# Performance work log

Measured on AMD Instinct MI355X. Metric: run time of the kernel, lower is better.

## Reference

```python
import jax, jax.numpy as jnp
import numpy as np
import math

B, S, D, H = 4, 2048, 1024, 16
DH = D // H  # 64


def setup_inputs() -> dict:
    key = jax.random.key(0)
    ks = jax.random.split(key, 7)
    scale = 1.0 / math.sqrt(D)
    q = jax.random.normal(ks[0], (B, S, D), dtype=jnp.float32)
    k = jax.random.normal(ks[1], (B, S, D), dtype=jnp.float32)
    v = jax.random.normal(ks[2], (B, S, D), dtype=jnp.float32)
    mask = jnp.tril(jnp.ones((S, S), dtype=jnp.int32))[None, None]  # [1,1,S,S] causal
    wq = jax.random.normal(ks[3], (D, D), dtype=jnp.float32) * scale
    wk = jax.random.normal(ks[4], (D, D), dtype=jnp.float32) * scale
    wv = jax.random.normal(ks[5], (D, D), dtype=jnp.float32) * scale
    wo = jax.random.normal(ks[6], (D, D), dtype=jnp.float32) * scale
    return {"q": q, "k": k, "v": v, "mask": mask, "wq": wq, "wk": wk, "wv": wv, "wo": wo}


def reference(q, k, v, mask, wq, wk, wv, wo):
    # nn.Linear(bias=False): y = x @ W.T
    qry = q @ wq.T
    key = k @ wk.T
    val = v @ wv.T
    # [B,S,D] -> [B,H,S,DH]
    qry = qry.reshape(B, S, H, DH).transpose(0, 2, 1, 3)
    key = key.reshape(B, S, H, DH).transpose(0, 2, 1, 3)
    val = val.reshape(B, S, H, DH).transpose(0, 2, 1, 3)
    scores = jnp.einsum('bhqd,bhkd->bhqk', qry, key) / math.sqrt(DH)
    scores = jnp.where(mask == 0, jnp.float32(-1e9), scores)
    attn = jax.nn.softmax(scores, axis=-1)  # dropout p=0.0 -> identity
    x = jnp.einsum('bhqk,bhkd->bhqd', attn, val)
    x = x.transpose(0, 2, 1, 3).reshape(B, S, D)
    return x @ wo.T
```

## Files before the change

### kernel.cpp

```cpp
#include <hip/hip_runtime.h>
#include <hip/hip_bf16.h>

typedef __attribute__((ext_vector_type(8))) short bf16x8;
typedef __attribute__((ext_vector_type(4))) float f32x4;
typedef __attribute__((ext_vector_type(16))) float f32x16;

#define MFMA16(a, b, c) __builtin_amdgcn_mfma_f32_16x16x32_bf16((a), (b), (c), 0, 0, 0)
#define MFMA32(a, b, c) __builtin_amdgcn_mfma_f32_32x32x16_bf16((a), (b), (c), 0, 0, 0)

#if defined(__has_builtin)
#if __has_builtin(__builtin_amdgcn_exp2f)
#define EXP2(x) __builtin_amdgcn_exp2f(x)
#endif
#endif
#ifndef EXP2
#define EXP2(x) exp2f(x)
#endif

__device__ __forceinline__ short f2b(float f) {
  unsigned u = __builtin_bit_cast(unsigned, f);
  u += 0x7FFFu + ((u >> 16) & 1u);
  return (short)(u >> 16);
}
__device__ __forceinline__ unsigned cvtpk(float lo, float hi) {
  unsigned r;
  asm("v_cvt_pk_bf16_f32 %0, %1, %2" : "=v"(r) : "v"(lo), "v"(hi));
  return r;
}

__global__ __launch_bounds__(256) void cvt_bf16(const float* __restrict__ s,
                                                short* __restrict__ d, int n8) {
  int i = blockIdx.x * 256 + threadIdx.x;
  if (i >= n8) return;
  const float4* sp = (const float4*)s;
  float4 a = sp[2 * i], b = sp[2 * i + 1];
  bf16x8 o;
  o[0] = f2b(a.x); o[1] = f2b(a.y); o[2] = f2b(a.z); o[3] = f2b(a.w);
  o[4] = f2b(b.x); o[5] = f2b(b.y); o[6] = f2b(b.z); o[7] = f2b(b.w);
  *(bf16x8*)(d + (long)i * 8) = o;
}

template <int MODE>
__global__ __launch_bounds__(256) void gemm_bt(const short* __restrict__ A,
                                               const short* __restrict__ BT,
                                               void* __restrict__ Cout,
                                               int M, int N, int K, float oscale) {
  __shared__ __align__(16) short As[128 * 64];
  __shared__ __align__(16) short Bs[128 * 64];
  const int t = threadIdx.x;
  const int l = t & 63, w = t >> 6;
  const int grp = l >> 4, li = l & 15;
  const int nbn = N >> 7;
  const int bm = (int)blockIdx.x / nbn, bn = (int)blockIdx.x % nbn;
  const int m0 = bm << 7, n0 = bn << 7;
  const int wm = (w >> 1) << 6, wn = (w & 1) << 6;
  const int srow = t >> 3, scol = (t & 7) << 3;
  f32x4 acc[4][4] = {};
  for (int kt = 0; kt < K; kt += 64) {
#pragma unroll
    for (int i = 0; i < 4; ++i) {
      const short* ga = A + (long)(m0 + i * 32 + srow) * K + kt + scol;
      __builtin_amdgcn_global_load_lds(
          (const __attribute__((address_space(1))) void*)ga,
          (__attribute__((address_space(3))) void*)&As[i * 2048 + t * 8], 16, 0, 0);
    }
#pragma unroll
    for (int i = 0; i < 4; ++i) {
      const short* gb = BT + (long)(n0 + i * 32 + srow) * K + kt + scol;
      __builtin_amdgcn_global_load_lds(
          (const __attribute__((address_space(1))) void*)gb,
          (__attribute__((address_space(3))) void*)&Bs[i * 2048 + t * 8], 16, 0, 0);
    }
    __syncthreads();
#pragma unroll
    for (int kk = 0; kk < 64; kk += 32) {
      bf16x8 af[4], bfr[4];
#pragma unroll
      for (int mi = 0; mi < 4; ++mi)
        af[mi] = *(const bf16x8*)&As[(wm + mi * 16 + li) * 64 + kk + grp * 8];
#pragma unroll
      for (int ni = 0; ni < 4; ++ni)
        bfr[ni] = *(const bf16x8*)&Bs[(wn + ni * 16 + li) * 64 + kk + grp * 8];
#pragma unroll
      for (int mi = 0; mi < 4; ++mi)
#pragma unroll
        for (int ni = 0; ni < 4; ++ni)
          acc[mi][ni] = MFMA16(af[mi], bfr[ni], acc[mi][ni]);
    }
    __syncthreads();
  }
#pragma unroll
  for (int mi = 0; mi < 4; ++mi) {
#pragma unroll
    for (int ni = 0; ni < 4; ++ni) {
      f32x4 v = acc[mi][ni];
      int n = n0 + wn + ni * 16 + li;
#pragma unroll
      for (int r = 0; r < 4; ++r) {
        int m = m0 + wm + mi * 16 + grp * 4 + r;
        if (MODE == 2) {
          ((float*)Cout)[(long)m * N + n] = v[r];
        } else {
          int b = m >> 11, sq = m & 2047;
          int h = n >> 6, dh = n & 63;
          if (MODE == 0)
            ((short*)Cout)[(((long)(b * 16 + h) * 2048 + sq) << 6) + dh] = f2b(v[r] * oscale);
          else
            ((short*)Cout)[(((long)(b * 16 + h) * 64 + dh) << 11) + sq] = f2b(v[r] * oscale);
        }
      }
    }
  }
}

__device__ __forceinline__ void attn_tile(const short* Kbuf, const short* Vbuf,
                                          const bf16x8 qf[4], f32x16& oa, f32x16& ob,
                                          float& mrun, float& lsum, int kt, bool diag,
                                          int khmax, int qg, int q, int hi) {
  f32x16 p0 = {}, p1 = {};
  __builtin_amdgcn_s_setprio(1);
#pragma unroll
  for (int kd = 0; kd < 4; ++kd) {
    int colB = kd * 32 + hi * 16;
    bf16x8 kf0 = *(const bf16x8*)((const char*)Kbuf + q * 128 + (colB ^ ((q & 7) << 4)));
    p0 = MFMA32(kf0, qf[kd], p0);
  }
  if (khmax == 2) {
#pragma unroll
    for (int kd = 0; kd < 4; ++kd) {
      int colB = kd * 32 + hi * 16;
      bf16x8 kf1 = *(const bf16x8*)((const char*)Kbuf + (q + 32) * 128 + (colB ^ ((q & 7) << 4)));
      p1 = MFMA32(kf1, qf[kd], p1);
    }
  }
  __builtin_amdgcn_s_setprio(0);
  if (diag) {
#pragma unroll
    for (int r = 0; r < 16; ++r) {
      int key0 = kt * 64 + (r & 3) + 8 * (r >> 2) + 4 * hi;
      if (key0 > qg) p0[r] = -1e30f;
      if (key0 + 32 > qg) p1[r] = -1e30f;
    }
  }
  float pm = p0[0];
#pragma unroll
  for (int r = 1; r < 16; ++r) pm = fmaxf(pm, p0[r]);
  if (khmax == 2) {
#pragma unroll
    for (int r = 0; r < 16; ++r) pm = fmaxf(pm, p1[r]);
  }
  pm = fmaxf(pm, __shfl_xor(pm, 32));
  const bool skip = __all(pm - mrun <= 11.5f);
  float mn;
  float alpha = 1.f;
  if (skip) {
    mn = mrun;
  } else {
    mn = fmaxf(mrun, pm);
    alpha = EXP2(mrun - mn);
    mrun = mn;
  }
  float ts = 0.f;
#pragma unroll
  for (int r = 0; r < 16; ++r) { p0[r] = EXP2(p0[r] - mn); ts += p0[r]; }
  if (khmax == 2) {
#pragma unroll
    for (int r = 0; r < 16; ++r) { p1[r] = EXP2(p1[r] - mn); ts += p1[r]; }
  }
  ts += __shfl_xor(ts, 32);
  if (skip) {
    lsum += ts;
  } else {
    lsum = lsum * alpha + ts;
#pragma unroll
    for (int r = 0; r < 16; ++r) { oa[r] *= alpha; ob[r] *= alpha; }
  }
  unsigned own0[8], prt0[8], own1[8], prt1[8];
#pragma unroll
  for (int g = 0; g < 4; ++g) {
    own0[2 * g]     = cvtpk(p0[4 * g], p0[4 * g + 1]);
    own0[2 * g + 1] = cvtpk(p0[4 * g + 2], p0[4 * g + 3]);
  }
#pragma unroll
  for (int i = 0; i < 8; ++i) prt0[i] = __shfl_xor(own0[i], 32);
  if (khmax == 2) {
#pragma unroll
    for (int g = 0; g < 4; ++g) {
      own1[2 * g]     = cvtpk(p1[4 * g], p1[4 * g + 1]);
      own1[2 * g + 1] = cvtpk(p1[4 * g + 2], p1[4 * g + 3]);
    }
#pragma unroll
    for (int i = 0; i < 8; ++i) prt1[i] = __shfl_xor(own1[i], 32);
  }
  __builtin_amdgcn_s_setprio(1);
#define PVSTEP(KD, OWN, PRT)                                                              \
  {                                                                                       \
    const int kdl = (KD) & 1;                                                             \
    unsigned b0 = hi ? PRT[4 * kdl + 2] : OWN[4 * kdl];                                   \
    unsigned b1 = hi ? PRT[4 * kdl + 3] : OWN[4 * kdl + 1];                               \
    unsigned b2 = hi ? OWN[4 * kdl + 2] : PRT[4 * kdl];                                   \
    unsigned b3 = hi ? OWN[4 * kdl + 3] : PRT[4 * kdl + 1];                               \
    int4 bi = {(int)b0, (int)b1, (int)b2, (int)b3};                                       \
    bf16x8 pb = __builtin_bit_cast(bf16x8, bi);                                           \
    int colB = (KD) * 32 + hi * 16;                                                       \
    bf16x8 vf0 = *(const bf16x8*)((const char*)Vbuf + q * 128 + (colB ^ ((q & 7) << 4))); \
    bf16x8 vf1 = *(const bf16x8*)((const char*)Vbuf + (q + 32) * 128 + (colB ^ ((q & 7) << 4))); \
    oa = MFMA32(vf0, pb, oa);                                                             \
    ob = MFMA32(vf1, pb, ob);                                                             \
  }
  PVSTEP(0, own0, prt0);
  PVSTEP(1, own0, prt0);
  if (khmax == 2) {
    PVSTEP(2, own1, prt1);
    PVSTEP(3, own1, prt1);
  }
#undef PVSTEP
  __builtin_amdgcn_s_setprio(0);
}

__global__ __launch_bounds__(256, 2) void attn_fwd(const short* __restrict__ Qh,
                                                   const short* __restrict__ Kh,
                                                   const short* __restrict__ Vt,
                                                   short* __restrict__ Xb) {
  __shared__ __align__(16) short Ks[2][4096];
  __shared__ __align__(16) short Vs[2][4096];
  const int bh = blockIdx.x;
  const int qtA = blockIdx.y;
  const int qtB = 15 - qtA;
  const int t = threadIdx.x, l = t & 63, w = t >> 6;
  const int q = l & 31, hi = l >> 5;
  const int q0wA = qtA * 128 + w * 32, q0wB = qtB * 128 + w * 32;
  const int qgA = q0wA + q, qgB = q0wB + q;
  const short* Qp = Qh + (long)bh * 131072;
  const char* Kb = (const char*)(Kh + (long)bh * 131072);
  const char* Vb = (const char*)(Vt + (long)bh * 131072);

  bf16x8 qfA[4], qfB[4];
#pragma unroll
  for (int kd = 0; kd < 4; ++kd) {
    qfA[kd] = *(const bf16x8*)(Qp + (long)qgA * 64 + kd * 16 + hi * 8);
    qfB[kd] = *(const bf16x8*)(Qp + (long)qgB * 64 + kd * 16 + hi * 8);
  }

  const int co0 = t * 16, co1 = co0 + 4096;

  f32x16 oaA = {}, obA = {}, oaB = {}, obB = {};
  float mrunA = -1e30f, lsumA = 0.f, mrunB = -1e30f, lsumB = 0.f;
  const int tripsA = (q0wA >> 6) + 1;
  const int tripsB = (q0wB >> 6) + 1;
  const int nt = 2 * qtB + 2;

#define STAGE(KT, BUF)                                                                   \
  {                                                                                      \
    long ktb = (long)(KT) * 8192;                                                        \
    _Pragma("unroll") for (int c = 0; c < 2; ++c) {                                      \
      int o = c ? co1 : co0;                                                             \
      int ksrc = o ^ (((o >> 7) & 7) << 4);                                              \
      __builtin_amdgcn_global_load_lds(                                                  \
          (const __attribute__((address_space(1))) void*)(Kb + ktb + ksrc),              \
          (__attribute__((address_space(3))) void*)((char*)Ks[BUF] + o), 16, 0, 0);      \
      int row = o >> 7, c16 = (o >> 4) & 7;                                              \
      int vsrc = row * 4096 + (KT) * 128 + (((c16 ^ (row & 7))) << 4);                   \
      __builtin_amdgcn_global_load_lds(                                                  \
          (const __attribute__((address_space(1))) void*)(Vb + vsrc),                    \
          (__attribute__((address_space(3))) void*)((char*)Vs[BUF] + o), 16, 0, 0);      \
    }                                                                                    \
  }

  STAGE(0, 0);
  __syncthreads();

  for (int kt = 0; kt < nt; ++kt) {
    const int buf = kt & 1;
    if (kt + 1 < nt) STAGE(kt + 1, buf ^ 1);

    if (kt < tripsB) {
      const bool diag = (kt == tripsB - 1);
      const int khmax = (diag && ((q0wB & 32) == 0)) ? 1 : 2;
      attn_tile(Ks[buf], Vs[buf], qfB, oaB, obB, mrunB, lsumB, kt, diag, khmax, qgB, q, hi);
    }
    if (kt < tripsA) {
      const bool diag = (kt == tripsA - 1);
      const int khmax = (diag && ((q0wA & 32) == 0)) ? 1 : 2;
      attn_tile(Ks[buf], Vs[buf], qfA, oaA, obA, mrunA, lsumA, kt, diag, khmax, qgA, q, hi);
    }
    __syncthreads();
  }

  const int b = bh >> 4, h = bh & 15;
#define EPI(OA, OB, LS, QG)                                                \
  {                                                                        \
    const float inv = 1.f / (LS);                                          \
    short* orow = Xb + (long)(b * 2048 + (QG)) * 1024 + h * 64;            \
    _Pragma("unroll") for (int g = 0; g < 4; ++g) {                        \
      unsigned u0 = cvtpk((OA)[4 * g] * inv, (OA)[4 * g + 1] * inv);       \
      unsigned u1 = cvtpk((OA)[4 * g + 2] * inv, (OA)[4 * g + 3] * inv);   \
      uint2 uu = {u0, u1};                                                 \
      *(uint2*)(orow + 8 * g + 4 * hi) = uu;                               \
      unsigned w0 = cvtpk((OB)[4 * g] * inv, (OB)[4 * g + 1] * inv);       \
      unsigned w1 = cvtpk((OB)[4 * g + 2] * inv, (OB)[4 * g + 3] * inv);   \
      uint2 ww = {w0, w1};                                                 \
      *(uint2*)(orow + 32 + 8 * g + 4 * hi) = ww;                          \
    }                                                                      \
  }
  EPI(oaA, obA, lsumA, qgA);
  EPI(oaB, obB, lsumB, qgB);
#undef EPI
}

extern "C" void kernel_launch(void* const* d_in, const int* in_sizes, int n_in,
                              void* d_out, int out_size, void* d_ws, size_t ws_size,
                              hipStream_t stream) {
  const float* q  = (const float*)d_in[0];
  const float* k  = (const float*)d_in[1];
  const float* v  = (const float*)d_in[2];
  const float* wq = (const float*)d_in[4];
  const float* wk = (const float*)d_in[5];
  const float* wv = (const float*)d_in[6];
  const float* wo = (const float*)d_in[7];

  short* ws = (short*)d_ws;
  const long T = 8388608;
  short* qb  = ws;
  short* kb  = qb + T;
  short* vb  = kb + T;
  short* Qh  = vb + T;
  short* Kh  = Qh + T;
  short* Vt  = Kh + T;
  short* Xb  = Vt + T;
  short* wqb = Xb + T;
  short* wkb = wqb + 1048576;
  short* wvb = wkb + 1048576;
  short* wob = wvb + 1048576;

  cvt_bf16<<<4096, 256, 0, stream>>>(q, qb, 1048576);
  cvt_bf16<<<4096, 256, 0, stream>>>(k, kb, 1048576);
  cvt_bf16<<<4096, 256, 0, stream>>>(v, vb, 1048576);
  cvt_bf16<<<512, 256, 0, stream>>>(wq, wqb, 131072);
  cvt_bf16<<<512, 256, 0, stream>>>(wk, wkb, 131072);
  cvt_bf16<<<512, 256, 0, stream>>>(wv, wvb, 131072);
  cvt_bf16<<<512, 256, 0, stream>>>(wo, wob, 131072);

  gemm_bt<0><<<512, 256, 0, stream>>>(qb, wqb, (void*)Qh, 8192, 1024, 1024, 0.18033688f);
  gemm_bt<0><<<512, 256, 0, stream>>>(kb, wkb, (void*)Kh, 8192, 1024, 1024, 1.0f);
  gemm_bt<1><<<512, 256, 0, stream>>>(vb, wvb, (void*)Vt, 8192, 1024, 1024, 1.0f);
  attn_fwd<<<dim3(64, 8), 256, 0, stream>>>(Qh, Kh, Vt, Xb);
  gemm_bt<2><<<512, 256, 0, stream>>>(Xb, wob, d_out, 8192, 1024, 1024, 1.0f);
}
```

Baseline: 223.8 us.

## Double-buffer GEMM LDS tiles and batch input conversion launches

The projection GEMM now keeps two LDS buffers and issues the global-to-LDS loads for the next K tile before computing on the current one, so memory latency overlaps with MFMA work. The seven separate fp32-to-bf16 conversion launches are merged into two launches that use blockIdx.y to select the source tensor. Together these aim to hide load stalls and cut launch overhead. In exchange, per-block LDS use doubles, which may reduce how many blocks fit per CU.

```diff
diff --git a/kernel.cpp b/kernel.cpp
--- a/kernel.cpp
+++ b/kernel.cpp
@@ -28,16 +28,34 @@
   return r;
 }
 
-__global__ __launch_bounds__(256) void cvt_bf16(const float* __restrict__ s,
-                                                short* __restrict__ d, int n8) {
-  int i = blockIdx.x * 256 + threadIdx.x;
-  if (i >= n8) return;
+__global__ __launch_bounds__(256) void cvt3_bf16(const float* __restrict__ s0,
+                                                 const float* __restrict__ s1,
+                                                 const float* __restrict__ s2,
+                                                 short* __restrict__ d, long stride) {
+  const int which = blockIdx.y;
+  const float* s = which == 0 ? s0 : (which == 1 ? s1 : s2);
+  long i = (long)blockIdx.x * 256 + threadIdx.x;
   const float4* sp = (const float4*)s;
   float4 a = sp[2 * i], b = sp[2 * i + 1];
   bf16x8 o;
   o[0] = f2b(a.x); o[1] = f2b(a.y); o[2] = f2b(a.z); o[3] = f2b(a.w);
   o[4] = f2b(b.x); o[5] = f2b(b.y); o[6] = f2b(b.z); o[7] = f2b(b.w);
-  *(bf16x8*)(d + (long)i * 8) = o;
+  *(bf16x8*)(d + which * stride + i * 8) = o;
+}
+__global__ __launch_bounds__(256) void cvt4_bf16(const float* __restrict__ s0,
+                                                 const float* __restrict__ s1,
+                                                 const float* __restrict__ s2,
+                                                 const float* __restrict__ s3,
+                                                 short* __restrict__ d, long stride) {
+  const int which = blockIdx.y;
+  const float* s = which == 0 ? s0 : (which == 1 ? s1 : (which == 2 ? s2 : s3));
+  long i = (long)blockIdx.x * 256 + threadIdx.x;
+  const float4* sp = (const float4*)s;
+  float4 a = sp[2 * i], b = sp[2 * i + 1];
+  bf16x8 o;
+  o[0] = f2b(a.x); o[1] = f2b(a.y); o[2] = f2b(a.z); o[3] = f2b(a.w);
+  o[4] = f2b(b.x); o[5] = f2b(b.y); o[6] = f2b(b.z); o[7] = f2b(b.w);
+  *(bf16x8*)(d + which * stride + i * 8) = o;
 }
 
 template <int MODE>
@@ -45,8 +63,8 @@
                                                const short* __restrict__ BT,
                                                void* __restrict__ Cout,
                                                int M, int N, int K, float oscale) {
-  __shared__ __align__(16) short As[128 * 64];
-  __shared__ __align__(16) short Bs[128 * 64];
+  __shared__ __align__(16) short As[2][128 * 64];
+  __shared__ __align__(16) short Bs[2][128 * 64];
   const int t = threadIdx.x;
   const int l = t & 63, w = t >> 6;
   const int grp = l >> 4, li = l & 15;
@@ -55,32 +73,39 @@
   const int m0 = bm << 7, n0 = bn << 7;
   const int wm = (w >> 1) << 6, wn = (w & 1) << 6;
   const int srow = t >> 3, scol = (t & 7) << 3;
+  const int NT = K >> 6;
   f32x4 acc[4][4] = {};
-  for (int kt = 0; kt < K; kt += 64) {
-#pragma unroll
-    for (int i = 0; i < 4; ++i) {
-      const short* ga = A + (long)(m0 + i * 32 + srow) * K + kt + scol;
-      __builtin_amdgcn_global_load_lds(
-          (const __attribute__((address_space(1))) void*)ga,
-          (__attribute__((address_space(3))) void*)&As[i * 2048 + t * 8], 16, 0, 0);
-    }
-#pragma unroll
-    for (int i = 0; i < 4; ++i) {
-      const short* gb = BT + (long)(n0 + i * 32 + srow) * K + kt + scol;
-      __builtin_amdgcn_global_load_lds(
-          (const __attribute__((address_space(1))) void*)gb,
-          (__attribute__((address_space(3))) void*)&Bs[i * 2048 + t * 8], 16, 0, 0);
-    }
-    __syncthreads();
+
+#define GSTAGE(KT, BUF)                                                                    \
+  {                                                                                        \
+    _Pragma("unroll") for (int i = 0; i < 4; ++i) {                                        \
+      const short* ga = A + (long)(m0 + i * 32 + srow) * K + (KT) * 64 + scol;             \
+      __builtin_amdgcn_global_load_lds(                                                    \
+          (const __attribute__((address_space(1))) void*)ga,                               \
+          (__attribute__((address_space(3))) void*)&As[BUF][i * 2048 + t * 8], 16, 0, 0);  \
+    }                                                                                      \
+    _Pragma("unroll") for (int i = 0; i < 4; ++i) {                                        \
+      const short* gb = BT + (long)(n0 + i * 32 + srow) * K + (KT) * 64 + scol;            \
+      __builtin_amdgcn_global_load_lds(                                                    \
+          (const __attribute__((address_space(1))) void*)gb,                               \
+          (__attribute__((address_space(3))) void*)&Bs[BUF][i * 2048 + t * 8], 16, 0, 0);  \
+    }                                                                                      \
+  }
+
+  GSTAGE(0, 0);
+  __syncthreads();
+  for (int kt = 0; kt < NT; ++kt) {
+    const int cur = kt & 1;
+    if (kt + 1 < NT) GSTAGE(kt + 1, cur ^ 1);
 #pragma unroll
     for (int kk = 0; kk < 64; kk += 32) {
       bf16x8 af[4], bfr[4];
 #pragma unroll
       for (int mi = 0; mi < 4; ++mi)
-        af[mi] = *(const bf16x8*)&As[(wm + mi * 16 + li) * 64 + kk + grp * 8];
+        af[mi] = *(const bf16x8*)&As[cur][(wm + mi * 16 + li) * 64 + kk + grp * 8];
 #pragma unroll
       for (int ni = 0; ni < 4; ++ni)
-        bfr[ni] = *(const bf16x8*)&Bs[(wn + ni * 16 + li) * 64 + kk + grp * 8];
+        bfr[ni] = *(const bf16x8*)&Bs[cur][(wn + ni * 16 + li) * 64 + kk + grp * 8];
 #pragma unroll
       for (int mi = 0; mi < 4; ++mi)
 #pragma unroll
@@ -89,6 +114,7 @@
     }
     __syncthreads();
   }
+#undef GSTAGE
 #pragma unroll
   for (int mi = 0; mi < 4; ++mi) {
 #pragma unroll
@@ -333,13 +359,8 @@
   short* wvb = wkb + 1048576;
   short* wob = wvb + 1048576;
 
-  cvt_bf16<<<4096, 256, 0, stream>>>(q, qb, 1048576);
-  cvt_bf16<<<4096, 256, 0, stream>>>(k, kb, 1048576);
-  cvt_bf16<<<4096, 256, 0, stream>>>(v, vb, 1048576);
-  cvt_bf16<<<512, 256, 0, stream>>>(wq, wqb, 131072);
-  cvt_bf16<<<512, 256, 0, stream>>>(wk, wkb, 131072);
-  cvt_bf16<<<512, 256, 0, stream>>>(wv, wvb, 131072);
-  cvt_bf16<<<512, 256, 0, stream>>>(wo, wob, 131072);
+  cvt3_bf16<<<dim3(4096, 3), 256, 0, stream>>>(q, k, v, qb, T);
+  cvt4_bf16<<<dim3(512, 4), 256, 0, stream>>>(wq, wk, wv, wo, wqb, 1048576);
 
   gemm_bt<0><<<512, 256, 0, stream>>>(qb, wqb, (void*)Qh, 8192, 1024, 1024, 0.18033688f);
   gemm_bt<0><<<512, 256, 0, stream>>>(kb, wkb, (void*)Kh, 8192, 1024, 1024, 1.0f);
```

Result: faster. 216.1 us (-3.5%).
